# Performance work log

Measured on AMD Instinct MI355X. Metric: run time of the kernel, lower is better.

Reference implementation:

```python
import jax, jax.numpy as jnp
import numpy as np

# static config (must match init_kwargs / input_specs)
N = 100000; E = 1600000; IN_DIM = 128; D = 64
H = 16; S = 8; MAX_STEP = 3; G = 512
PEN = 128; C = 10; BN_EPS = 1e-5
F_OUT = MAX_STEP * H * S  # 384


def setup_inputs() -> dict:
    key = jax.random.key(0)
    ks = jax.random.split(key, 16)
    inp = {}
    inp['x'] = jax.random.normal(ks[0], (N, IN_DIM), dtype=jnp.float32)
    inp['edge_index'] = jax.random.randint(ks[1], (2, E), 0, N, dtype=jnp.int64 if jax.config.jax_enable_x64 else jnp.int32)
    inp['batch'] = jnp.sort(jax.random.randint(ks[2], (N,), 0, G, dtype=jnp.int64 if jax.config.jax_enable_x64 else jnp.int32))
    # learned params
    inp['adj_hidden'] = jax.random.uniform(ks[3], (H, S * (S - 1) // 2), minval=-1.0, maxval=1.0, dtype=jnp.float32)
    inp['features_hidden'] = jax.random.uniform(ks[4], (H, S, D), minval=0.0, maxval=1.0, dtype=jnp.float32)
    inp['fc_w'] = jax.random.normal(ks[5], (D, IN_DIM), dtype=jnp.float32) * 0.05
    inp['fc_b'] = jnp.zeros((D,), jnp.float32)
    inp['rw_w'] = jax.random.normal(ks[6], (MAX_STEP - 1, D, D), dtype=jnp.float32) * 0.05
    inp['rw_b'] = jnp.zeros((MAX_STEP - 1, D), jnp.float32)
    inp['bn_gamma'] = jnp.ones((F_OUT,), jnp.float32)
    inp['bn_beta'] = jnp.zeros((F_OUT,), jnp.float32)
    inp['fc1_w'] = jax.random.normal(ks[7], (PEN, F_OUT), dtype=jnp.float32) * 0.05
    inp['fc1_b'] = jnp.zeros((PEN,), jnp.float32)
    inp['fc2_w'] = jax.random.normal(ks[8], (C, PEN), dtype=jnp.float32) * 0.05
    inp['fc2_b'] = jnp.zeros((C,), jnp.float32)
    return inp


def _rwconv(x, row, col, w, b):
    # RWConv: add self-loops, deg over row, out[col] += (1/deg[row]) * x[row], then Linear
    sl = jnp.arange(N, dtype=row.dtype)
    r = jnp.concatenate([row, sl])
    c = jnp.concatenate([col, sl])
    deg = jax.ops.segment_sum(jnp.ones_like(r, x.dtype), r, num_segments=N)
    dinv = jnp.where(deg > 0, 1.0 / deg, 0.0)
    msg = dinv[r][:, None] * x[r]              # [E+N, D]
    agg = jax.ops.segment_sum(msg, c, num_segments=N)  # [N, D]
    return agg @ w.T + b


def reference(x, edge_index, batch, adj_hidden, features_hidden, fc_w, fc_b,
              rw_w, rw_b, bn_gamma, bn_beta, fc1_w, fc1_b, fc2_w, fc2_b):
    row, col = edge_index[0], edge_index[1]
    # symmetric hidden adjacency from relu'd upper-triangular params
    iu, ju = np.triu_indices(S, 1)
    A = jnp.zeros((H, S, S), x.dtype).at[:, iu, ju].set(jax.nn.relu(adj_hidden))
    A = A + jnp.transpose(A, (0, 2, 1))

    xh = jax.nn.sigmoid(x @ fc_w.T + fc_b)     # [N, D]
    z = features_hidden                         # [H, S, D]
    zx = jnp.einsum('hsd,nd->hsn', z, xh)       # [H, S, N]

    outs = []
    cur = xh
    for i in range(MAX_STEP):
        if i == 0:
            t = zx                              # eye @ z == z
        else:
            cur = _rwconv(cur, row, col, rw_w[i - 1], rw_b[i - 1])
            z = jnp.einsum('hab,hbd->had', A, z)
            t = jnp.einsum('hsd,nd->hsn', z, cur)
        t = zx * t                              # [H, S, N]  (dropout p=0)
        # fused segment-reduce over nodes -> graph buckets (replaces per-node loop)
        tg = jax.ops.segment_sum(jnp.transpose(t, (2, 0, 1)), batch, num_segments=G)  # [G, H, S]
        t_graphs = jnp.transpose(tg, (1, 2, 0))             # [H, S, G]
        t2 = jnp.transpose(t_graphs, (1, 2, 0))             # transpose(0,1) then (1,2) -> [S, G, H]
        outs.append(t2.reshape(G, -1))                      # faithful reshape(n_graphs, -1)
    out = jnp.concatenate(outs, axis=1)                     # [G, MAX_STEP*S*H]

    # BatchNorm1d (fresh module => training-mode batch statistics)
    mean = out.mean(axis=0)
    var = out.var(axis=0)
    out = (out - mean) / jnp.sqrt(var + BN_EPS) * bn_gamma + bn_beta

    out = jax.nn.relu(out @ fc1_w.T + fc1_b)
    out = out @ fc2_w.T + fc2_b
    return jax.nn.log_softmax(out, axis=1)
```

## Files before the change

kernel.cpp:

```cpp
#include <hip/hip_runtime.h>
#include <stdint.h>

#define N_NODES 100000
#define E_EDGES 1600000
#define INDIM 128
#define DD 64
#define HH 16
#define SS 8
#define HS 128
#define GG 512
#define PENN 128
#define CC 10
#define F_OUT 384
#define BN_EPS 1e-5f
#define NBLK_SCAN ((N_NODES + 255)/256)
#define GSPLIT 8

__global__ void k_init_deg(float* deg){
    int n = blockIdx.x*256 + threadIdx.x;
    if(n < N_NODES) deg[n] = 1.0f;
}

__global__ void k_deg(const int* __restrict__ row, float* deg){
    int e = blockIdx.x*256 + threadIdx.x;
    if(e < E_EDGES) atomicAdd(&deg[row[e]], 1.0f);
}

__global__ void k_zero_cnt(int* cnt){
    int n = blockIdx.x*256 + threadIdx.x;
    if(n < N_NODES) cnt[n] = 0;
}

__global__ void k_hist(const int* __restrict__ col, int* __restrict__ cnt){
    int e = blockIdx.x*256 + threadIdx.x;
    if(e < E_EDGES) atomicAdd(&cnt[col[e]], 1);
}

__global__ void k_scan_bsum(const int* __restrict__ cnt, int* __restrict__ bsum){
    int b = blockIdx.x, t = threadIdx.x, i = b*256 + t;
    int v = (i < N_NODES) ? cnt[i] : 0;
    #pragma unroll
    for(int off = 32; off; off >>= 1) v += __shfl_down(v, off);
    __shared__ int ws[4];
    if((t & 63) == 0) ws[t >> 6] = v;
    __syncthreads();
    if(t == 0) bsum[b] = ws[0] + ws[1] + ws[2] + ws[3];
}

__global__ __launch_bounds__(512) void k_scan_boff(const int* __restrict__ bsum,
                                                   int* __restrict__ boff,
                                                   int* __restrict__ rowptr){
    __shared__ int buf[512];
    int t = threadIdx.x;
    int v = (t < NBLK_SCAN) ? bsum[t] : 0;
    buf[t] = v;
    __syncthreads();
    for(int off = 1; off < 512; off <<= 1){
        int add = (t >= off) ? buf[t - off] : 0;
        __syncthreads();
        buf[t] += add;
        __syncthreads();
    }
    if(t < NBLK_SCAN) boff[t] = buf[t] - v;
    if(t == 0) rowptr[N_NODES] = buf[511];
}

__global__ void k_scan_final(const int* __restrict__ cnt, const int* __restrict__ boff,
                             int* __restrict__ rowptr, int* __restrict__ cursor){
    int b = blockIdx.x, t = threadIdx.x, i = b*256 + t;
    int lane = t & 63, w = t >> 6;
    int v = (i < N_NODES) ? cnt[i] : 0;
    int x = v;
    #pragma unroll
    for(int off = 1; off < 64; off <<= 1){
        int y = __shfl_up(x, off);
        if(lane >= off) x += y;
    }
    __shared__ int wsum[4];
    if(lane == 63) wsum[w] = x;
    __syncthreads();
    int wpre = 0;
    #pragma unroll
    for(int k = 0; k < 4; ++k) wpre += (k < w) ? wsum[k] : 0;
    int excl = boff[b] + wpre + x - v;
    if(i < N_NODES){ rowptr[i] = excl; cursor[i] = excl; }
}

__global__ void k_fill(const int* __restrict__ row, const int* __restrict__ col,
                       int* __restrict__ cursor, int* __restrict__ erow){
    int e = blockIdx.x*256 + threadIdx.x;
    if(e < E_EDGES){
        int idx = atomicAdd(&cursor[col[e]], 1);
        erow[idx] = row[e];
    }
}

__global__ __launch_bounds__(256) void k_xh(const float* __restrict__ x, const float* __restrict__ fc_w,
                     const float* __restrict__ fc_b, const float* __restrict__ deg,
                     float* __restrict__ xh, float* __restrict__ ybuf){
    __shared__ float xl[8][INDIM];
    int tid  = threadIdx.x;
    int lane = tid & 63;
    int wv   = tid >> 6;
    float w[INDIM];
    const float4* wr = (const float4*)(fc_w + (size_t)lane*INDIM);
    #pragma unroll
    for(int q = 0; q < INDIM/4; ++q){
        float4 v = wr[q];
        w[4*q+0] = v.x; w[4*q+1] = v.y; w[4*q+2] = v.z; w[4*q+3] = v.w;
    }
    float bias = fc_b[lane];
    int r = tid >> 5, q0 = tid & 31;
    #pragma unroll 1
    for(int base = blockIdx.x*8; base < N_NODES; base += gridDim.x*8){
        __syncthreads();
        int nn = base + r;
        float4 v = (nn < N_NODES) ? ((const float4*)(x + (size_t)nn*INDIM))[q0]
                                  : make_float4(0.f,0.f,0.f,0.f);
        ((float4*)xl[r])[q0] = v;
        __syncthreads();
        #pragma unroll
        for(int j = 0; j < 2; ++j){
            int n = base + wv*2 + j;
            if(n < N_NODES){
                const float4* cp = (const float4*)xl[wv*2 + j];
                float a0 = 0.f, a1 = 0.f, a2 = 0.f, a3 = 0.f;
                #pragma unroll
                for(int q = 0; q < INDIM/4; q += 4){
                    float4 v0 = cp[q], v1 = cp[q+1], v2 = cp[q+2], v3 = cp[q+3];
                    a0 = fmaf(v0.x, w[4*q+ 0], a0); a0 = fmaf(v0.y, w[4*q+ 1], a0);
                    a0 = fmaf(v0.z, w[4*q+ 2], a0); a0 = fmaf(v0.w, w[4*q+ 3], a0);
                    a1 = fmaf(v1.x, w[4*q+ 4], a1); a1 = fmaf(v1.y, w[4*q+ 5], a1);
                    a1 = fmaf(v1.z, w[4*q+ 6], a1); a1 = fmaf(v1.w, w[4*q+ 7], a1);
                    a2 = fmaf(v2.x, w[4*q+ 8], a2); a2 = fmaf(v2.y, w[4*q+ 9], a2);
                    a2 = fmaf(v2.z, w[4*q+10], a2); a2 = fmaf(v2.w, w[4*q+11], a2);
                    a3 = fmaf(v3.x, w[4*q+12], a3); a3 = fmaf(v3.y, w[4*q+13], a3);
                    a3 = fmaf(v3.z, w[4*q+14], a3); a3 = fmaf(v3.w, w[4*q+15], a3);
                }
                float acc = bias + ((a0 + a1) + (a2 + a3));
                float s = 1.0f/(1.0f + expf(-acc));
                size_t o = (size_t)n*DD + lane;
                xh[o] = s;
                ybuf[o] = s / deg[n];
            }
        }
    }
}

__global__ __launch_bounds__(256) void k_gather(const int* __restrict__ rowptr, const int* __restrict__ erow,
                        const float* __restrict__ y, float* __restrict__ agg){
    int lane = threadIdx.x & 63;
    int wave = (blockIdx.x*256 + threadIdx.x) >> 6;
    int nwaves = gridDim.x * 4;
    #pragma unroll 1
    for(int n = wave; n < N_NODES; n += nwaves){
        int b = rowptr[n], en = rowptr[n+1];
        float acc = y[(size_t)n*DD + lane];
        #pragma unroll 2
        for(int j = b; j < en; ++j){
            int rr = erow[j];
            acc += y[(size_t)rr*DD + lane];
        }
        agg[(size_t)n*DD + lane] = acc;
    }
}

__global__ __launch_bounds__(256) void k_lin(const float* __restrict__ agg, const float* __restrict__ w_,
                     const float* __restrict__ b, const float* __restrict__ deg,
                     float* __restrict__ cur, float* __restrict__ ynext, int make_next){
    int lane = threadIdx.x & 63;
    int wave = (blockIdx.x*256 + threadIdx.x) >> 6;
    int nwaves = gridDim.x * 4;
    float w[DD];
    const float4* wr = (const float4*)(w_ + (size_t)lane*DD);
    #pragma unroll
    for(int q = 0; q < DD/4; ++q){
        float4 v = wr[q];
        w[4*q+0] = v.x; w[4*q+1] = v.y; w[4*q+2] = v.z; w[4*q+3] = v.w;
    }
    float bias = b[lane];
    #pragma unroll 1
    for(int n = wave; n < N_NODES; n += nwaves){
        const float4* ar = (const float4*)(agg + (size_t)n*DD);
        float acc = bias;
        #pragma unroll
        for(int q = 0; q < DD/4; ++q){
            float4 v = ar[q];
            acc = fmaf(v.x, w[4*q+0], acc);
            acc = fmaf(v.y, w[4*q+1], acc);
            acc = fmaf(v.z, w[4*q+2], acc);
            acc = fmaf(v.w, w[4*q+3], acc);
        }
        size_t o = (size_t)n*DD + lane;
        cur[o] = acc;
        if(make_next) ynext[o] = acc / deg[n];
    }
}

__global__ void k_adj(const float* __restrict__ adj_hidden,
                      float* __restrict__ A1g, float* __restrict__ A2g){
    __shared__ float A[HH][SS][SS];
    int tid = threadIdx.x;
    for(int i = tid; i < HH*SS*SS; i += 256) ((float*)A)[i] = 0.0f;
    __syncthreads();
    for(int i = tid; i < HH*28; i += 256){
        int h = i / 28, p = i % 28;
        int iu = 0, ju = 0, cnt = 0;
        for(int a = 0; a < SS-1; ++a){
            int rl = SS-1-a;
            if(p < cnt + rl){ iu = a; ju = a + 1 + (p - cnt); break; }
            cnt += rl;
        }
        float v = adj_hidden[i];
        v = v > 0.f ? v : 0.f;
        A[h][iu][ju] = v;
        A[h][ju][iu] = v;
    }
    __syncthreads();
    for(int i = tid; i < HH*SS*SS; i += 256){
        int h = i >> 6, s = (i >> 3) & 7, b = i & 7;
        A1g[i] = A[h][s][b];
        float acc = 0.f;
        #pragma unroll
        for(int k = 0; k < SS; ++k) acc += A[h][s][k] * A[h][k][b];
        A2g[i] = acc;
    }
}

__global__ void k_bounds(const int* __restrict__ batch, int* __restrict__ start){
    int n = blockIdx.x*256 + threadIdx.x;
    if(n >= N_NODES) return;
    int b = batch[n];
    int prev = (n == 0) ? -1 : batch[n-1];
    for(int g = prev + 1; g <= b; ++g) start[g] = n;
    if(n == N_NODES-1){
        for(int g = b + 1; g <= GG; ++g) start[g] = N_NODES;
    }
}

__global__ void k_zero_P(float* P){
    int i = blockIdx.x*256 + threadIdx.x;
    if(i < 3*GG*HS) P[i] = 0.f;
}

__global__ __launch_bounds__(256) void k_feat(const float* __restrict__ z0,
                      const float* __restrict__ A1g, const float* __restrict__ A2g,
                      const float* __restrict__ xh, const float* __restrict__ cur1,
                      const float* __restrict__ cur2,
                      const int* __restrict__ start, float* __restrict__ P){
    __shared__ float xhl[8][DD];
    __shared__ float c1l[8][DD];
    __shared__ float c2l[8][DD];
    __shared__ float red[HS][3];
    int tid  = threadIdx.x;
    int lane = tid & 63;
    int hs   = tid & 127;
    int slot = tid >> 7;
    int g = blockIdx.x / GSPLIT;
    int q = blockIdx.x - g*GSPLIT;
    int s0 = start[g], s1 = start[g+1];

    float zr[DD];
    {
        const float4* zp = (const float4*)(z0 + (size_t)hs*DD);
        #pragma unroll
        for(int qq = 0; qq < 16; ++qq){
            float4 v = zp[qq];
            zr[4*qq+0]=v.x; zr[4*qq+1]=v.y; zr[4*qq+2]=v.z; zr[4*qq+3]=v.w;
        }
    }
    float a1r[8], a2r[8];
    #pragma unroll
    for(int b = 0; b < 8; ++b){
        a1r[b] = A1g[hs*8 + b];
        a2r[b] = A2g[hs*8 + b];
    }

    float acc0 = 0.f, acc1 = 0.f, acc2 = 0.f;
    #pragma unroll 1
    for(int base = s0 + q*8; base < s1; base += 8*GSPLIT){
        __syncthreads();
        #pragma unroll
        for(int k = 0; k < 2; ++k){
            int idx = tid + k*256;
            int nn = base + (idx >> 6);
            int d  = idx & 63;
            bool ok = nn < s1;
            size_t off = (size_t)nn*DD + d;
            xhl[idx >> 6][d] = ok ? xh  [off] : 0.f;
            c1l[idx >> 6][d] = ok ? cur1[off] : 0.f;
            c2l[idx >> 6][d] = ok ? cur2[off] : 0.f;
        }
        __syncthreads();
        #pragma unroll
        for(int j = 0; j < 4; ++j){
            int n = base + slot*4 + j;
            if(n < s1){
                const float4* xp = (const float4*)(xhl[slot*4 + j]);
                const float4* p1 = (const float4*)(c1l[slot*4 + j]);
                const float4* p2 = (const float4*)(c2l[slot*4 + j]);
                float zx = 0.f, u1 = 0.f, u2 = 0.f;
                #pragma unroll
                for(int qq = 0; qq < 16; ++qq){
                    float4 a = xp[qq], b = p1[qq], c = p2[qq];
                    zx = fmaf(a.x, zr[4*qq+0], zx);
                    zx = fmaf(a.y, zr[4*qq+1], zx);
                    zx = fmaf(a.z, zr[4*qq+2], zx);
                    zx = fmaf(a.w, zr[4*qq+3], zx);
                    u1 = fmaf(b.x, zr[4*qq+0], u1);
                    u1 = fmaf(b.y, zr[4*qq+1], u1);
                    u1 = fmaf(b.z, zr[4*qq+2], u1);
                    u1 = fmaf(b.w, zr[4*qq+3], u1);
                    u2 = fmaf(c.x, zr[4*qq+0], u2);
                    u2 = fmaf(c.y, zr[4*qq+1], u2);
                    u2 = fmaf(c.z, zr[4*qq+2], u2);
                    u2 = fmaf(c.w, zr[4*qq+3], u2);
                }
                float dt1 = 0.f, dt2 = 0.f;
                int gb = lane & 56;
                #pragma unroll
                for(int b = 0; b < 8; ++b){
                    float v1 = __shfl(u1, gb + b);
                    float v2 = __shfl(u2, gb + b);
                    dt1 = fmaf(a1r[b], v1, dt1);
                    dt2 = fmaf(a2r[b], v2, dt2);
                }
                acc0 = fmaf(zx, zx,  acc0);
                acc1 = fmaf(zx, dt1, acc1);
                acc2 = fmaf(zx, dt2, acc2);
            }
        }
    }
    __syncthreads();
    if(slot == 1){ red[hs][0] = acc0; red[hs][1] = acc1; red[hs][2] = acc2; }
    __syncthreads();
    if(slot == 0){
        atomicAdd(&P[(size_t)0*GG*HS + (size_t)g*HS + hs], acc0 + red[hs][0]);
        atomicAdd(&P[(size_t)1*GG*HS + (size_t)g*HS + hs], acc1 + red[hs][1]);
        atomicAdd(&P[(size_t)2*GG*HS + (size_t)g*HS + hs], acc2 + red[hs][2]);
    }
}

__global__ void k_outpre(const float* __restrict__ P, float* __restrict__ outp){
    int idx = blockIdx.x*256 + threadIdx.x;
    if(idx >= GG*F_OUT) return;
    int r = idx / F_OUT, j = idx % F_OUT;
    int i = j >> 7, c = j & 127;
    int g = ((r & 63) << 3) + (c >> 4);
    int h = c & 15, s = r >> 6;
    int hs = h*SS + s;
    outp[idx] = P[((size_t)i*GG + g)*HS + hs];
}

__global__ void k_bnstats(const float* __restrict__ outp, const float* __restrict__ gamma,
                          const float* __restrict__ beta, float* __restrict__ scale_,
                          float* __restrict__ shift_){
    int j = blockIdx.x;
    int t = threadIdx.x;
    float v[8];
    float sum = 0.f;
    #pragma unroll
    for(int i = 0; i < 8; ++i){ v[i] = outp[(size_t)(t*8+i)*F_OUT + j]; sum += v[i]; }
    #pragma unroll
    for(int off = 32; off; off >>= 1) sum += __shfl_down(sum, off);
    sum = __shfl(sum, 0);
    float mean = sum / (float)GG;
    float sq = 0.f;
    #pragma unroll
    for(int i = 0; i < 8; ++i){ float d = v[i] - mean; sq = fmaf(d, d, sq); }
    #pragma unroll
    for(int off = 32; off; off >>= 1) sq += __shfl_down(sq, off);
    if(t == 0){
        float var = sq / (float)GG;
        float rstd = rsqrtf(var + BN_EPS);
        float sc = rstd * gamma[j];
        scale_[j] = sc;
        shift_[j] = beta[j] - mean*sc;
    }
}

__global__ __launch_bounds__(128) void k_mlp(const float* __restrict__ outp, const float* __restrict__ scale_,
                     const float* __restrict__ shift_, const float* __restrict__ fc1w,
                     const float* __restrict__ fc1b, const float* __restrict__ fc2w,
                     const float* __restrict__ fc2b, float* __restrict__ out){
    __shared__ float nrm[F_OUT];
    __shared__ float hid[PENN];
    __shared__ float logit[CC];
    int r = blockIdx.x, t = threadIdx.x;
    for(int j = t; j < F_OUT; j += 128)
        nrm[j] = fmaf(outp[(size_t)r*F_OUT + j], scale_[j], shift_[j]);
    __syncthreads();
    float acc = fc1b[t];
    #pragma unroll 8
    for(int j = 0; j < F_OUT; ++j) acc = fmaf(nrm[j], fc1w[(size_t)t*F_OUT + j], acc);
    hid[t] = acc > 0.f ? acc : 0.f;
    __syncthreads();
    if(t < CC){
        float a = fc2b[t];
        #pragma unroll
        for(int p = 0; p < PENN; ++p) a = fmaf(hid[p], fc2w[t*PENN + p], a);
        logit[t] = a;
    }
    __syncthreads();
    if(t < CC){
        float m = logit[0];
        #pragma unroll
        for(int c = 1; c < CC; ++c) m = fmaxf(m, logit[c]);
        float se = 0.f;
        #pragma unroll
        for(int c = 0; c < CC; ++c) se += expf(logit[c] - m);
        out[r*CC + t] = logit[t] - m - logf(se);
    }
}

extern "C" void kernel_launch(void* const* d_in, const int* in_sizes, int n_in,
                              void* d_out, int out_size, void* d_ws, size_t ws_size,
                              hipStream_t stream){
    const float* x      = (const float*)d_in[0];
    const int*   edges  = (const int*)d_in[1];
    const int*   batch  = (const int*)d_in[2];
    const float* adjh   = (const float*)d_in[3];
    const float* fh     = (const float*)d_in[4];
    const float* fc_w   = (const float*)d_in[5];
    const float* fc_b   = (const float*)d_in[6];
    const float* rw_w   = (const float*)d_in[7];
    const float* rw_b   = (const float*)d_in[8];
    const float* gamma  = (const float*)d_in[9];
    const float* beta   = (const float*)d_in[10];
    const float* fc1w   = (const float*)d_in[11];
    const float* fc1b   = (const float*)d_in[12];
    const float* fc2w   = (const float*)d_in[13];
    const float* fc2b   = (const float*)d_in[14];
    float* out = (float*)d_out;

    const int* row = edges;
    const int* col = edges + E_EDGES;

    size_t off = 0;
    auto alloc_f = [&](size_t nf) -> float* {
        float* p = (float*)((char*)d_ws + off);
        off += nf * sizeof(float);
        off = (off + 255) & ~(size_t)255;
        return p;
    };
    float* deg    = alloc_f(N_NODES);
    float* xh     = alloc_f((size_t)N_NODES*DD);
    float* ybuf   = alloc_f((size_t)N_NODES*DD);
    float* agg1   = alloc_f((size_t)N_NODES*DD);
    float* agg2   = alloc_f((size_t)N_NODES*DD);
    float* cur1   = alloc_f((size_t)N_NODES*DD);
    float* cur2   = alloc_f((size_t)N_NODES*DD);
    float* A1g    = alloc_f(HH*SS*SS);
    float* A2g    = alloc_f(HH*SS*SS);
    float* P      = alloc_f((size_t)3*GG*HS);
    float* outp   = alloc_f((size_t)GG*F_OUT);
    float* scl    = alloc_f(F_OUT);
    float* shf    = alloc_f(F_OUT);
    int*   start  = (int*)alloc_f(GG + 1);
    int*   cnt    = (int*)alloc_f(N_NODES);
    int*   rowptr = (int*)alloc_f(N_NODES + 1);
    int*   cursor = (int*)alloc_f(N_NODES);
    int*   bsum   = (int*)alloc_f(NBLK_SCAN);
    int*   boff   = (int*)alloc_f(NBLK_SCAN);
    int*   erow   = (int*)alloc_f(E_EDGES);

    int blkN = (N_NODES + 255)/256;
    int blkE = (E_EDGES + 255)/256;

    k_init_deg<<<blkN, 256, 0, stream>>>(deg);
    k_deg<<<blkE, 256, 0, stream>>>(row, deg);
    k_zero_cnt<<<blkN, 256, 0, stream>>>(cnt);
    k_hist<<<blkE, 256, 0, stream>>>(col, cnt);
    k_scan_bsum<<<NBLK_SCAN, 256, 0, stream>>>(cnt, bsum);
    k_scan_boff<<<1, 512, 0, stream>>>(bsum, boff, rowptr);
    k_scan_final<<<NBLK_SCAN, 256, 0, stream>>>(cnt, boff, rowptr, cursor);
    k_fill<<<blkE, 256, 0, stream>>>(row, col, cursor, erow);

    k_xh<<<1024, 256, 0, stream>>>(x, fc_w, fc_b, deg, xh, ybuf);
    k_gather<<<1024, 256, 0, stream>>>(rowptr, erow, ybuf, agg1);
    k_lin<<<1024, 256, 0, stream>>>(agg1, rw_w, rw_b, deg, cur1, ybuf, 1);
    k_gather<<<1024, 256, 0, stream>>>(rowptr, erow, ybuf, agg2);
    k_lin<<<1024, 256, 0, stream>>>(agg2, rw_w + DD*DD, rw_b + DD, deg, cur2, nullptr, 0);

    k_adj<<<1, 256, 0, stream>>>(adjh, A1g, A2g);
    k_bounds<<<blkN, 256, 0, stream>>>(batch, start);
    k_zero_P<<<(3*GG*HS + 255)/256, 256, 0, stream>>>(P);
    k_feat<<<GSPLIT*GG, 256, 0, stream>>>(fh, A1g, A2g, xh, cur1, cur2, start, P);
    k_outpre<<<(GG*F_OUT + 255)/256, 256, 0, stream>>>(P, outp);
    k_bnstats<<<F_OUT, 64, 0, stream>>>(outp, gamma, beta, scl, shf);
    k_mlp<<<GG, 128, 0, stream>>>(outp, scl, shf, fc1w, fc1b, fc2w, fc2b, out);
}
```

Measured before the change: 1.063 ms.

## Fuse gather with linear layer, merge degree/histogram kernels, double-buffer feature staging

Merges the row-degree and column-histogram passes into one edge kernel using integer counts, and drops the separate float degree buffer. Fuses each gather-aggregate pass with the following 64x64 linear layer through a per-wave LDS buffer, so the intermediate agg arrays are no longer written and re-read. Double-buffers the node staging in the feature kernel so the next tile's loads are issued before the current tile is computed. The fused kernel relies on __threadfence_block for intra-wave LDS visibility instead of a barrier, and launches twice as many blocks.

```diff
diff --git a/kernel.cpp b/kernel.cpp
--- a/kernel.cpp
+++ b/kernel.cpp
@@ -16,24 +16,18 @@
 #define NBLK_SCAN ((N_NODES + 255)/256)
 #define GSPLIT 8
 
-__global__ void k_init_deg(float* deg){
+__global__ void k_zero_cnts(int* cnt_row, int* cnt_col){
     int n = blockIdx.x*256 + threadIdx.x;
-    if(n < N_NODES) deg[n] = 1.0f;
-}
-
-__global__ void k_deg(const int* __restrict__ row, float* deg){
+    if(n < N_NODES){ cnt_row[n] = 0; cnt_col[n] = 0; }
+}
+
+__global__ void k_deg_hist(const int* __restrict__ row, const int* __restrict__ col,
+                           int* __restrict__ cnt_row, int* __restrict__ cnt_col){
     int e = blockIdx.x*256 + threadIdx.x;
-    if(e < E_EDGES) atomicAdd(&deg[row[e]], 1.0f);
-}
-
-__global__ void k_zero_cnt(int* cnt){
-    int n = blockIdx.x*256 + threadIdx.x;
-    if(n < N_NODES) cnt[n] = 0;
-}
-
-__global__ void k_hist(const int* __restrict__ col, int* __restrict__ cnt){
-    int e = blockIdx.x*256 + threadIdx.x;
-    if(e < E_EDGES) atomicAdd(&cnt[col[e]], 1);
+    if(e < E_EDGES){
+        atomicAdd(&cnt_row[row[e]], 1);
+        atomicAdd(&cnt_col[col[e]], 1);
+    }
 }
 
 __global__ void k_scan_bsum(const int* __restrict__ cnt, int* __restrict__ bsum){
@@ -96,7 +90,7 @@
 }
 
 __global__ __launch_bounds__(256) void k_xh(const float* __restrict__ x, const float* __restrict__ fc_w,
-                     const float* __restrict__ fc_b, const float* __restrict__ deg,
+                     const float* __restrict__ fc_b, const int* __restrict__ cnt_row,
                      float* __restrict__ xh, float* __restrict__ ybuf){
     __shared__ float xl[8][INDIM];
     int tid  = threadIdx.x;
@@ -141,34 +135,19 @@
                 float s = 1.0f/(1.0f + expf(-acc));
                 size_t o = (size_t)n*DD + lane;
                 xh[o] = s;
-                ybuf[o] = s / deg[n];
+                ybuf[o] = s / (float)(cnt_row[n] + 1);
             }
         }
     }
 }
 
-__global__ __launch_bounds__(256) void k_gather(const int* __restrict__ rowptr, const int* __restrict__ erow,
-                        const float* __restrict__ y, float* __restrict__ agg){
+__global__ __launch_bounds__(256) void k_gather_lin(const int* __restrict__ rowptr, const int* __restrict__ erow,
+                        const float* __restrict__ y, const float* __restrict__ w_,
+                        const float* __restrict__ b, const int* __restrict__ cnt_row,
+                        float* __restrict__ cur, float* __restrict__ ynext, int make_next){
+    __shared__ float aggl[4][DD];
     int lane = threadIdx.x & 63;
-    int wave = (blockIdx.x*256 + threadIdx.x) >> 6;
-    int nwaves = gridDim.x * 4;
-    #pragma unroll 1
-    for(int n = wave; n < N_NODES; n += nwaves){
-        int b = rowptr[n], en = rowptr[n+1];
-        float acc = y[(size_t)n*DD + lane];
-        #pragma unroll 2
-        for(int j = b; j < en; ++j){
-            int rr = erow[j];
-            acc += y[(size_t)rr*DD + lane];
-        }
-        agg[(size_t)n*DD + lane] = acc;
-    }
-}
-
-__global__ __launch_bounds__(256) void k_lin(const float* __restrict__ agg, const float* __restrict__ w_,
-                     const float* __restrict__ b, const float* __restrict__ deg,
-                     float* __restrict__ cur, float* __restrict__ ynext, int make_next){
-    int lane = threadIdx.x & 63;
+    int wv   = threadIdx.x >> 6;
     int wave = (blockIdx.x*256 + threadIdx.x) >> 6;
     int nwaves = gridDim.x * 4;
     float w[DD];
@@ -181,19 +160,30 @@
     float bias = b[lane];
     #pragma unroll 1
     for(int n = wave; n < N_NODES; n += nwaves){
-        const float4* ar = (const float4*)(agg + (size_t)n*DD);
-        float acc = bias;
-        #pragma unroll
-        for(int q = 0; q < DD/4; ++q){
-            float4 v = ar[q];
-            acc = fmaf(v.x, w[4*q+0], acc);
-            acc = fmaf(v.y, w[4*q+1], acc);
-            acc = fmaf(v.z, w[4*q+2], acc);
-            acc = fmaf(v.w, w[4*q+3], acc);
-        }
+        int bb = rowptr[n], en = rowptr[n+1];
+        float acc = y[(size_t)n*DD + lane];
+        #pragma unroll 2
+        for(int j = bb; j < en; ++j){
+            int rr = erow[j];
+            acc += y[(size_t)rr*DD + lane];
+        }
+        aggl[wv][lane] = acc;
+        __threadfence_block();
+        const float4* ap = (const float4*)aggl[wv];
+        float a0 = 0.f, a1 = 0.f;
+        #pragma unroll
+        for(int q = 0; q < DD/4; q += 2){
+            float4 v0 = ap[q], v1 = ap[q+1];
+            a0 = fmaf(v0.x, w[4*q+0], a0); a0 = fmaf(v0.y, w[4*q+1], a0);
+            a0 = fmaf(v0.z, w[4*q+2], a0); a0 = fmaf(v0.w, w[4*q+3], a0);
+            a1 = fmaf(v1.x, w[4*q+4], a1); a1 = fmaf(v1.y, w[4*q+5], a1);
+            a1 = fmaf(v1.z, w[4*q+6], a1); a1 = fmaf(v1.w, w[4*q+7], a1);
+        }
+        float outv = bias + a0 + a1;
         size_t o = (size_t)n*DD + lane;
-        cur[o] = acc;
-        if(make_next) ynext[o] = acc / deg[n];
+        cur[o] = outv;
+        if(make_next) ynext[o] = outv / (float)(cnt_row[n] + 1);
+        __threadfence_block();
     }
 }
 
@@ -248,9 +238,9 @@
                       const float* __restrict__ xh, const float* __restrict__ cur1,
                       const float* __restrict__ cur2,
                       const int* __restrict__ start, float* __restrict__ P){
-    __shared__ float xhl[8][DD];
-    __shared__ float c1l[8][DD];
-    __shared__ float c2l[8][DD];
+    __shared__ float xhl[2][8][DD];
+    __shared__ float c1l[2][8][DD];
+    __shared__ float c2l[2][8][DD];
     __shared__ float red[HS][3];
     int tid  = threadIdx.x;
     int lane = tid & 63;
@@ -259,6 +249,7 @@
     int g = blockIdx.x / GSPLIT;
     int q = blockIdx.x - g*GSPLIT;
     int s0 = start[g], s1 = start[g+1];
+    const int STEP = 8*GSPLIT;
 
     float zr[DD];
     {
@@ -276,10 +267,7 @@
         a2r[b] = A2g[hs*8 + b];
     }
 
-    float acc0 = 0.f, acc1 = 0.f, acc2 = 0.f;
-    #pragma unroll 1
-    for(int base = s0 + q*8; base < s1; base += 8*GSPLIT){
-        __syncthreads();
+    auto stage = [&](int base, int buf){
         #pragma unroll
         for(int k = 0; k < 2; ++k){
             int idx = tid + k*256;
@@ -287,18 +275,28 @@
             int d  = idx & 63;
             bool ok = nn < s1;
             size_t off = (size_t)nn*DD + d;
-            xhl[idx >> 6][d] = ok ? xh  [off] : 0.f;
-            c1l[idx >> 6][d] = ok ? cur1[off] : 0.f;
-            c2l[idx >> 6][d] = ok ? cur2[off] : 0.f;
-        }
+            xhl[buf][idx >> 6][d] = ok ? xh  [off] : 0.f;
+            c1l[buf][idx >> 6][d] = ok ? cur1[off] : 0.f;
+            c2l[buf][idx >> 6][d] = ok ? cur2[off] : 0.f;
+        }
+    };
+
+    float acc0 = 0.f, acc1 = 0.f, acc2 = 0.f;
+    int first = s0 + q*8;
+    int cur = 0;
+    if(first < s1) stage(first, 0);
+    #pragma unroll 1
+    for(int base = first; base < s1; base += STEP){
         __syncthreads();
+        int nb = base + STEP;
+        if(nb < s1) stage(nb, cur ^ 1);
         #pragma unroll
         for(int j = 0; j < 4; ++j){
             int n = base + slot*4 + j;
             if(n < s1){
-                const float4* xp = (const float4*)(xhl[slot*4 + j]);
-                const float4* p1 = (const float4*)(c1l[slot*4 + j]);
-                const float4* p2 = (const float4*)(c2l[slot*4 + j]);
+                const float4* xp = (const float4*)(xhl[cur][slot*4 + j]);
+                const float4* p1 = (const float4*)(c1l[cur][slot*4 + j]);
+                const float4* p2 = (const float4*)(c2l[cur][slot*4 + j]);
                 float zx = 0.f, u1 = 0.f, u2 = 0.f;
                 #pragma unroll
                 for(int qq = 0; qq < 16; ++qq){
@@ -330,6 +328,7 @@
                 acc2 = fmaf(zx, dt2, acc2);
             }
         }
+        cur ^= 1;
     }
     __syncthreads();
     if(slot == 1){ red[hs][0] = acc0; red[hs][1] = acc1; red[hs][2] = acc2; }
@@ -443,11 +442,9 @@
         off = (off + 255) & ~(size_t)255;
         return p;
     };
-    float* deg    = alloc_f(N_NODES);
     float* xh     = alloc_f((size_t)N_NODES*DD);
     float* ybuf   = alloc_f((size_t)N_NODES*DD);
-    float* agg1   = alloc_f((size_t)N_NODES*DD);
-    float* agg2   = alloc_f((size_t)N_NODES*DD);
+    float* ybuf2  = alloc_f((size_t)N_NODES*DD);
     float* cur1   = alloc_f((size_t)N_NODES*DD);
     float* cur2   = alloc_f((size_t)N_NODES*DD);
     float* A1g    = alloc_f(HH*SS*SS);
@@ -457,7 +454,8 @@
     float* scl    = alloc_f(F_OUT);
     float* shf    = alloc_f(F_OUT);
     int*   start  = (int*)alloc_f(GG + 1);
-    int*   cnt    = (int*)alloc_f(N_NODES);
+    int*   cnt_r  = (int*)alloc_f(N_NODES);
+    int*   cnt_c  = (int*)alloc_f(N_NODES);
     int*   rowptr = (int*)alloc_f(N_NODES + 1);
     int*   cursor = (int*)alloc_f(N_NODES);
     int*   bsum   = (int*)alloc_f(NBLK_SCAN);
@@ -467,20 +465,16 @@
     int blkN = (N_NODES + 255)/256;
     int blkE = (E_EDGES + 255)/256;
 
-    k_init_deg<<<blkN, 256, 0, stream>>>(deg);
-    k_deg<<<blkE, 256, 0, stream>>>(row, deg);
-    k_zero_cnt<<<blkN, 256, 0, stream>>>(cnt);
-    k_hist<<<blkE, 256, 0, stream>>>(col, cnt);
-    k_scan_bsum<<<NBLK_SCAN, 256, 0, stream>>>(cnt, bsum);
+    k_zero_cnts<<<blkN, 256, 0, stream>>>(cnt_r, cnt_c);
+    k_deg_hist<<<blkE, 256, 0, stream>>>(row, col, cnt_r, cnt_c);
+    k_scan_bsum<<<NBLK_SCAN, 256, 0, stream>>>(cnt_c, bsum);
     k_scan_boff<<<1, 512, 0, stream>>>(bsum, boff, rowptr);
-    k_scan_final<<<NBLK_SCAN, 256, 0, stream>>>(cnt, boff, rowptr, cursor);
+    k_scan_final<<<NBLK_SCAN, 256, 0, stream>>>(cnt_c, boff, rowptr, cursor);
     k_fill<<<blkE, 256, 0, stream>>>(row, col, cursor, erow);
 
-    k_xh<<<1024, 256, 0, stream>>>(x, fc_w, fc_b, deg, xh, ybuf);
-    k_gather<<<1024, 256, 0, stream>>>(rowptr, erow, ybuf, agg1);
-    k_lin<<<1024, 256, 0, stream>>>(agg1, rw_w, rw_b, deg, cur1, ybuf, 1);
-    k_gather<<<1024, 256, 0, stream>>>(rowptr, erow, ybuf, agg2);
-    k_lin<<<1024, 256, 0, stream>>>(agg2, rw_w + DD*DD, rw_b + DD, deg, cur2, nullptr, 0);
+    k_xh<<<1024, 256, 0, stream>>>(x, fc_w, fc_b, cnt_r, xh, ybuf);
+    k_gather_lin<<<2048, 256, 0, stream>>>(rowptr, erow, ybuf,  rw_w,         rw_b,      cnt_r, cur1, ybuf2, 1);
+    k_gather_lin<<<2048, 256, 0, stream>>>(rowptr, erow, ybuf2, rw_w + DD*DD, rw_b + DD, cnt_r, cur2, nullptr, 0);
 
     k_adj<<<1, 256, 0, stream>>>(adjh, A1g, A2g);
     k_bounds<<<blkN, 256, 0, stream>>>(batch, start);
```

After: 959.6 us. -9.7%, faster.
